# Optimization experiments

Hardware: AMD Instinct MI355X
Metric: run time of the kernel (lower is better)

## Reference

```python
import jax, jax.numpy as jnp
import numpy as np


def setup_inputs() -> dict:
    key = jax.random.key(0)
    k_y, k_cb = jax.random.split(key)
    B, C, H, W = 8, 192, 64, 64
    G, K = 8, 512
    d = C // G  # 24
    y = jax.random.normal(k_y, (B, C, H, W), dtype=jnp.float32)
    codebooks = jax.random.normal(k_cb, (G, K, d), dtype=jnp.float32)
    return {"y": y, "codebooks": codebooks}


def reference(y, codebooks):
    # y: [B, C, H, W]; codebooks: [G, K, d] with C == G*d
    B, C, H, W = y.shape
    G, K, d = codebooks.shape
    # split channels into G groups of dim d -> vectors at each spatial pos
    x = y.reshape(B, G, d, H, W).transpose(0, 3, 4, 1, 2)  # [B,H,W,G,d]
    x2 = jnp.sum(x * x, axis=-1, keepdims=True)            # [B,H,W,G,1]
    e2 = jnp.sum(codebooks * codebooks, axis=-1)           # [G,K]
    xe = jnp.einsum('bhwgd,gkd->bhwgk', x, codebooks)      # [B,H,W,G,K]
    dist = x2 - 2.0 * xe + e2                              # [B,H,W,G,K]
    idx = jnp.argmin(dist, axis=-1)                        # [B,H,W,G] int
    # gather quantized vectors per group (to_feather)
    q = codebooks[jnp.arange(G), idx]                      # [B,H,W,G,d]
    y_ba = q.transpose(0, 3, 4, 1, 2).reshape(B, C, H, W)  # [B,C,H,W]
    code_index = idx.transpose(0, 3, 1, 2)                 # [B,G,H,W]
    # straight-through estimator
    universal_ctx = y + jax.lax.stop_gradient(y_ba - y)
    return universal_ctx, y_ba, code_index[:, None]        # [B,1,G,H,W]
```

## Files before the change

kernel.cpp:

```cpp
#include <hip/hip_runtime.h>

#define B_   8
#define C_   192
#define HW_  4096
#define G_   8
#define K_   512
#define D_   24
#define CBSZ (K_ * D_)
#define THREADS 1024
#define NBLOCKS 512

#define LDS_HW   16384
#define WS_G_HW  16384

typedef float  f32x4 __attribute__((ext_vector_type(4)));
typedef int    i32x4 __attribute__((ext_vector_type(4)));
typedef short  s16x8 __attribute__((ext_vector_type(8)));
typedef short  s16x4 __attribute__((ext_vector_type(4)));
typedef _Float16 h16x8 __attribute__((ext_vector_type(8)));
typedef unsigned long long u64;

static __device__ __forceinline__ unsigned umin_(unsigned a, unsigned b){return a<b?a:b;}
static __device__ __forceinline__ unsigned umax_(unsigned a, unsigned b){return a>b?a:b;}
static __device__ __forceinline__ int dec_id(unsigned idb){
    return (int)((idb & 0x1F0u) | ((idb & 3u) << 2) | ((idb >> 2) & 3u));
}
static __device__ __forceinline__ unsigned pkrtz(float a, float b){
    return __builtin_bit_cast(unsigned, __builtin_amdgcn_cvt_pkrtz(a, b));
}
static __device__ __forceinline__ float lo16f(unsigned w){
    return (float)__builtin_bit_cast(_Float16, (unsigned short)(w & 0xFFFFu));
}
static __device__ __forceinline__ float hi16f(unsigned w){
    return (float)__builtin_bit_cast(_Float16, (unsigned short)(w >> 16));
}

__global__ __launch_bounds__(256) void vq_stage(
    const float* __restrict__ cb, unsigned short* __restrict__ ws)
{
    const int g = blockIdx.x >> 3;
    const int s = blockIdx.x & 7;
    const int tid = threadIdx.x;
    const float* cbg = cb + g * CBSZ;
    unsigned short* img = ws + g * WS_G_HW;

    for (int i = tid; i < 384; i += 256) {
        int gi = s * 384 + i;
        f32x4 v = ((const f32x4*)cbg)[gi];
        int i4 = gi << 2;
        int n  = i4 / 24;
        int k0 = i4 - n * 24;
        int off = (n >> 4) * 512 + (((k0 >> 3) << 4) + (n & 15)) * 8 + (k0 & 7);
        s16x4 h;
        #pragma unroll
        for (int j = 0; j < 4; ++j)
            h[j] = __builtin_bit_cast(short, (_Float16)v[j]);
        *(s16x4*)(&img[off]) = h;
    }
    if (tid < 64) {
        int n = s * 64 + tid;
        const float* row = cbg + n * D_;
        double s0 = 0.0, s1 = 0.0;
        #pragma unroll
        for (int j = 0; j < D_; j += 2) {
            double v0 = (double)row[j], v1 = (double)row[j+1];
            s0 = fma(v0,v0,s0); s1 = fma(v1,v1,s1);
        }
        double e2 = s0 + s1;
        _Float16 hi = (_Float16)(float)e2;
        _Float16 lo = (_Float16)(float)(e2 - (double)(float)hi);
        s16x8 pack = { __builtin_bit_cast(short, hi),
                       __builtin_bit_cast(short, lo), 0,0,0,0,0,0 };
        *(s16x8*)(&img[(n >> 4) * 512 + (48 + (n & 15)) * 8]) = pack;
    }
}

__global__ __launch_bounds__(THREADS, 8) void vq_main(
    const float* __restrict__ y, const float* __restrict__ cb,
    const unsigned short* __restrict__ ws, float* __restrict__ out)
{
    __shared__ __align__(16) unsigned short sB[LDS_HW];

    const int bid = blockIdx.x;
    const int g = bid & 7;
    const int blkg = bid >> 3;
    const int tid = threadIdx.x;
    const int wave = tid >> 6, lane = tid & 63;
    const int c = lane & 15, q = lane >> 4;

    const float* cbg = cb + g * CBSZ;

    {
        const char* src = (const char*)(ws + g * WS_G_HW);
        char* dst = (char*)sB;
        *(i32x4*)(dst + tid*16)         = *(const i32x4*)(src + tid*16);
        *(i32x4*)(dst + 16384 + tid*16) = *(const i32x4*)(src + 16384 + tid*16);
    }
    __syncthreads();

    float* out0 = out;
    float* out1 = out + B_*C_*HW_;
    float* out2 = out + 2*B_*C_*HW_;

    const unsigned short* aH = sB + lane * 8;

    const int wsid = (blkg << 4) + wave;
    const int hw    = (wsid & 255) << 4;
    const int bimg0 = wsid >> 8;
    int ybase[2];
    ybase[0] = (bimg0*C_ + g*D_)*HW_ + hw;
    ybase[1] = ybase[0] + 4*C_*HW_;

    h16x8 Xh[2], Xl[2];
    #pragma unroll
    for (int ti = 0; ti < 2; ++ti) {
        unsigned hx[4], lx[4];
        if (q < 3) {
            const float* yq = y + ybase[ti] + (q*8)*HW_ + c;
            float xf[8];
            #pragma unroll
            for (int jj = 0; jj < 8; ++jj) xf[jj] = -2.0f * yq[jj*HW_];
            #pragma unroll
            for (int p2 = 0; p2 < 4; ++p2) {
                float f0 = xf[2*p2], f1 = xf[2*p2+1];
                unsigned hw32 = pkrtz(f0, f1);
                float r0 = f0 - lo16f(hw32), r1 = f1 - hi16f(hw32);
                hx[p2] = hw32;
                lx[p2] = pkrtz(r0, r1);
            }
        } else {
            hx[0]=0x3C003C00u; hx[1]=0u; hx[2]=0u; hx[3]=0u;
            lx[0]=0u; lx[1]=0u; lx[2]=0u; lx[3]=0u;
        }
        Xh[ti] = __builtin_bit_cast(h16x8, (i32x4){(int)hx[0],(int)hx[1],(int)hx[2],(int)hx[3]});
        Xl[ti] = __builtin_bit_cast(h16x8, (i32x4){(int)lx[0],(int)lx[1],(int)lx[2],(int)lx[3]});
    }

    const f32x4 cbias = {128.0f, 128.0f, 128.0f, 128.0f};

    unsigned p1[2][4], p2[2][4];
    #pragma unroll
    for (int ti = 0; ti < 2; ++ti)
        #pragma unroll
        for (int r = 0; r < 4; ++r) { p1[ti][r] = ~0u; p2[ti][r] = ~0u; }

    #pragma unroll
    for (int t = 0; t < 32; ++t) {
        h16x8 eh = __builtin_bit_cast(h16x8, *(const s16x8*)(aH + t * 512));
        f32x4 a0 = __builtin_amdgcn_mfma_f32_16x16x32_f16(eh, Xh[0], cbias, 0,0,0);
        a0       = __builtin_amdgcn_mfma_f32_16x16x32_f16(eh, Xl[0], a0,   0,0,0);
        f32x4 a1 = __builtin_amdgcn_mfma_f32_16x16x32_f16(eh, Xh[1], cbias, 0,0,0);
        a1       = __builtin_amdgcn_mfma_f32_16x16x32_f16(eh, Xl[1], a1,   0,0,0);
        #pragma unroll
        for (int r = 0; r < 4; ++r) {
            {
                unsigned key = (__float_as_uint(a0[r]) & 0xFFFFFFE0u) | (unsigned)t;
                unsigned t2;
                asm("v_med3_u32 %0, %1, %2, %3" : "=v"(t2) : "v"(key), "v"(p1[0][r]), "v"(p2[0][r]));
                p2[0][r] = t2; p1[0][r] = umin_(p1[0][r], key);
            }
            {
                unsigned key = (__float_as_uint(a1[r]) & 0xFFFFFFE0u) | (unsigned)t;
                unsigned t2;
                asm("v_med3_u32 %0, %1, %2, %3" : "=v"(t2) : "v"(key), "v"(p1[1][r]), "v"(p2[1][r]));
                p2[1][r] = t2; p1[1][r] = umin_(p1[1][r], key);
            }
        }
    }

    #pragma unroll
    for (int ti = 0; ti < 2; ++ti) {
        unsigned s1[4], s2[4];
        #pragma unroll
        for (int r = 0; r < 4; ++r) {
            s1[r] = (p1[ti][r] << 2) | (unsigned)r;
            s2[r] = (p2[ti][r] << 2) | (unsigned)r;
        }
        unsigned A1,A2,A3, B1,B2,B3;
        {
            unsigned lo=umin_(s1[0],s1[1]), hi=umax_(s1[0],s1[1]);
            unsigned lo2=umin_(s2[0],s2[1]), hi2=umax_(s2[0],s2[1]);
            A1=lo; A2=umin_(hi,lo2); A3=umin_(umax_(hi,lo2),hi2);
        }
        {
            unsigned lo=umin_(s1[2],s1[3]), hi=umax_(s1[2],s1[3]);
            unsigned lo2=umin_(s2[2],s2[3]), hi2=umax_(s2[2],s2[3]);
            B1=lo; B2=umin_(hi,lo2); B3=umin_(umax_(hi,lo2),hi2);
        }
        unsigned w1=umin_(A1,B1), z1=umax_(A1,B1);
        unsigned w2=umin_(A2,B2), z2=umax_(A2,B2);
        unsigned w3=umin_(A3,B3);
        unsigned m1 = w1;
        unsigned m2 = umin_(z1,w2);
        unsigned m3 = umin_(umin_(umax_(z1,w2), z2), w3);

        unsigned b1 = (m1 << 2) | (unsigned)q;
        unsigned b2 = (m2 << 2) | (unsigned)q;
        unsigned b3 = (m3 << 2) | (unsigned)q;
        #pragma unroll
        for (int d = 16; d < 64; d <<= 1) {
            unsigned o1=__shfl_xor(b1,d,64), o2=__shfl_xor(b2,d,64), o3=__shfl_xor(b3,d,64);
            unsigned x = umax_(b1,o1);
            unsigned yv= umin_(b2,o2);
            unsigned w = umax_(b2,o2);
            unsigned z = umin_(b3,o3);
            b1 = umin_(b1,o1);
            b2 = umin_(x,yv);
            b3 = umin_(umax_(x,yv), umin_(w,z));
        }

        const int gap = (int)((b2 >> 9) - (b1 >> 9));
        int kwin;
        if (__ballot(gap < 64) == 0ull) {
            kwin = dec_id(b1 & 511u);
        } else {
            float xfr[8];
            if (q < 3) {
                const float* yq = y + ybase[ti] + (q*8)*HW_ + c;
                #pragma unroll
                for (int jj = 0; jj < 8; ++jj) xfr[jj] = -2.0f * yq[jj*HW_];
            } else {
                #pragma unroll
                for (int jj = 0; jj < 8; ++jj) xfr[jj] = 0.0f;
            }
            double xd[8];
            #pragma unroll
            for (int jj = 0; jj < 8; ++jj) xd[jj] = (double)xfr[jj];
            const unsigned cands[3] = {b1, b2, b3};
            u64 bestk = ~0ull;
            #pragma unroll
            for (int ci = 0; ci < 3; ++ci) {
                int kc = dec_id(cands[ci] & 511u);
                double s = 0.0;
                if (q < 3) {
                    const f32x4* ce4 = (const f32x4*)(cbg + kc*D_ + (q<<3));
                    float ef[8];
                    *(f32x4*)&ef[0] = ce4[0];
                    *(f32x4*)&ef[4] = ce4[1];
                    #pragma unroll
                    for (int jj = 0; jj < 8; ++jj) {
                        double ev = (double)ef[jj];
                        s = fma(ev, ev, s);
                        s = fma(xd[jj], ev, s);
                    }
                }
                s += __shfl_xor(s, 16, 64);
                s += __shfl_xor(s, 32, 64);
                s += 128.0;
                u64 kk = (((u64)__double_as_longlong(s)) & ~0x1FFull) | (u64)kc;
                bestk = kk < bestk ? kk : bestk;
            }
            kwin = (int)(bestk & 511ull);
        }

        const float* cw = cbg + kwin * D_;
        if (q < 3) {
            const f32x4* cw4 = (const f32x4*)(cw + (q<<3));
            float v[8];
            *(f32x4*)&v[0] = cw4[0];
            *(f32x4*)&v[4] = cw4[1];
            const int ob = ybase[ti] + (q*8)*HW_ + c;
            #pragma unroll
            for (int jj = 0; jj < 8; ++jj) {
                out0[ob + jj*HW_] = v[jj];
                out1[ob + jj*HW_] = v[jj];
            }
        }
        if (lane < 16) {
            const int bimg = bimg0 + 4*ti;
            out2[(bimg*G_ + g)*HW_ + hw + lane] = (float)kwin;
        }
    }
}

extern "C" void kernel_launch(void* const* d_in, const int* in_sizes, int n_in,
                              void* d_out, int out_size, void* d_ws, size_t ws_size,
                              hipStream_t stream) {
    const float* y  = (const float*)d_in[0];
    const float* cb = (const float*)d_in[1];
    float* out = (float*)d_out;
    unsigned short* ws = (unsigned short*)d_ws;

    vq_stage<<<dim3(64), dim3(256), 0, stream>>>(cb, ws);
    vq_main<<<dim3(NBLOCKS), dim3(THREADS), 0, stream>>>(y, cb, ws, out);
}
```

Measured before the change: 106.3 us.

## Add fp32 rescoring tier before fp64 fallback and widen codebook staging grid

When the top two fp16 candidates are close, the kernel now rescores the three candidates in fp32 using the already-held split-fp16 x values (Xh/Xl). It only falls back to reloading y and rescoring in fp64 when the fp32 margin between best and second is below a small threshold. This is meant to avoid the slow fp64 math and the extra global loads of y for most ambiguous pixels. The staging kernel is also spread over 256 smaller blocks instead of 64 so more CUs share the codebook conversion. The fp32 tier adds a ballot branch and depends on the chosen threshold being large enough to keep argmin results exact.

```diff
diff --git a/kernel.cpp b/kernel.cpp
--- a/kernel.cpp
+++ b/kernel.cpp
@@ -35,17 +35,17 @@
     return (float)__builtin_bit_cast(_Float16, (unsigned short)(w >> 16));
 }
 
-__global__ __launch_bounds__(256) void vq_stage(
+__global__ __launch_bounds__(128) void vq_stage(
     const float* __restrict__ cb, unsigned short* __restrict__ ws)
 {
-    const int g = blockIdx.x >> 3;
-    const int s = blockIdx.x & 7;
+    const int g = blockIdx.x >> 5;
+    const int s = blockIdx.x & 31;
     const int tid = threadIdx.x;
     const float* cbg = cb + g * CBSZ;
     unsigned short* img = ws + g * WS_G_HW;
 
-    for (int i = tid; i < 384; i += 256) {
-        int gi = s * 384 + i;
+    if (tid < 96) {
+        int gi = s * 96 + tid;
         f32x4 v = ((const f32x4*)cbg)[gi];
         int i4 = gi << 2;
         int n  = i4 / 24;
@@ -57,8 +57,8 @@
             h[j] = __builtin_bit_cast(short, (_Float16)v[j]);
         *(s16x4*)(&img[off]) = h;
     }
-    if (tid < 64) {
-        int n = s * 64 + tid;
+    if (tid < 16) {
+        int n = s * 16 + tid;
         const float* row = cbg + n * D_;
         double s0 = 0.0, s1 = 0.0;
         #pragma unroll
@@ -214,24 +214,12 @@
         if (__ballot(gap < 64) == 0ull) {
             kwin = dec_id(b1 & 511u);
         } else {
-            float xfr[8];
-            if (q < 3) {
-                const float* yq = y + ybase[ti] + (q*8)*HW_ + c;
-                #pragma unroll
-                for (int jj = 0; jj < 8; ++jj) xfr[jj] = -2.0f * yq[jj*HW_];
-            } else {
-                #pragma unroll
-                for (int jj = 0; jj < 8; ++jj) xfr[jj] = 0.0f;
-            }
-            double xd[8];
-            #pragma unroll
-            for (int jj = 0; jj < 8; ++jj) xd[jj] = (double)xfr[jj];
             const unsigned cands[3] = {b1, b2, b3};
-            u64 bestk = ~0ull;
+            unsigned kk[3];
             #pragma unroll
             for (int ci = 0; ci < 3; ++ci) {
                 int kc = dec_id(cands[ci] & 511u);
-                double s = 0.0;
+                float s = 0.0f;
                 if (q < 3) {
                     const f32x4* ce4 = (const f32x4*)(cbg + kc*D_ + (q<<3));
                     float ef[8];
@@ -239,18 +227,61 @@
                     *(f32x4*)&ef[4] = ce4[1];
                     #pragma unroll
                     for (int jj = 0; jj < 8; ++jj) {
-                        double ev = (double)ef[jj];
-                        s = fma(ev, ev, s);
-                        s = fma(xd[jj], ev, s);
+                        float xv = (float)Xh[ti][jj] + (float)Xl[ti][jj];
+                        s = fmaf(ef[jj], ef[jj], s);
+                        s = fmaf(xv, ef[jj], s);
                     }
                 }
                 s += __shfl_xor(s, 16, 64);
                 s += __shfl_xor(s, 32, 64);
-                s += 128.0;
-                u64 kk = (((u64)__double_as_longlong(s)) & ~0x1FFull) | (u64)kc;
-                bestk = kk < bestk ? kk : bestk;
-            }
-            kwin = (int)(bestk & 511ull);
+                s += 128.0f;
+                kk[ci] = (__float_as_uint(s) & 0xFFFFFE00u) | (unsigned)kc;
+            }
+            unsigned r1 = umin_(umin_(kk[0], kk[1]), kk[2]);
+            unsigned r2;
+            asm("v_med3_u32 %0, %1, %2, %3" : "=v"(r2) : "v"(kk[0]), "v"(kk[1]), "v"(kk[2]));
+            const float f1 = __uint_as_float(r1 & 0xFFFFFE00u);
+            const float f2 = __uint_as_float(r2 & 0xFFFFFE00u);
+            if (__ballot(f2 - f1 < 1.0e-3f) == 0ull) {
+                kwin = (int)(r1 & 511u);
+            } else {
+                float xfr[8];
+                if (q < 3) {
+                    const float* yq = y + ybase[ti] + (q*8)*HW_ + c;
+                    #pragma unroll
+                    for (int jj = 0; jj < 8; ++jj) xfr[jj] = -2.0f * yq[jj*HW_];
+                } else {
+                    #pragma unroll
+                    for (int jj = 0; jj < 8; ++jj) xfr[jj] = 0.0f;
+                }
+                double xd[8];
+                #pragma unroll
+                for (int jj = 0; jj < 8; ++jj) xd[jj] = (double)xfr[jj];
+                u64 bestk = ~0ull;
+                #pragma unroll
+                for (int ci = 0; ci < 3; ++ci) {
+                    int kc = dec_id(cands[ci] & 511u);
+                    double s = 0.0;
+                    if (q < 3) {
+                        const f32x4* ce4 = (const f32x4*)(cbg + kc*D_ + (q<<3));
+                        float ef[8];
+                        *(f32x4*)&ef[0] = ce4[0];
+                        *(f32x4*)&ef[4] = ce4[1];
+                        #pragma unroll
+                        for (int jj = 0; jj < 8; ++jj) {
+                            double ev = (double)ef[jj];
+                            s = fma(ev, ev, s);
+                            s = fma(xd[jj], ev, s);
+                        }
+                    }
+                    s += __shfl_xor(s, 16, 64);
+                    s += __shfl_xor(s, 32, 64);
+                    s += 128.0;
+                    u64 kv = (((u64)__double_as_longlong(s)) & ~0x1FFull) | (u64)kc;
+                    bestk = kv < bestk ? kv : bestk;
+                }
+                kwin = (int)(bestk & 511ull);
+            }
         }
 
         const float* cw = cbg + kwin * D_;
@@ -281,6 +312,6 @@
     float* out = (float*)d_out;
     unsigned short* ws = (unsigned short*)d_ws;
 
-    vq_stage<<<dim3(64), dim3(256), 0, stream>>>(cb, ws);
+    vq_stage<<<dim3(256), dim3(128), 0, stream>>>(cb, ws);
     vq_main<<<dim3(NBLOCKS), dim3(THREADS), 0, stream>>>(y, cb, ws, out);
 }
```

After: 109.1 us. 2.7% more time.
